# Kernel tuning notes

Measured on AMD Instinct MI355X. Metric: run time of the kernel, lower is better.

Reference implementation:

```python
import jax, jax.numpy as jnp
import numpy as np

T, B, D, H = 1024, 64, 128, 512
ALPHA = 10.0 / 100.0  # dt / tau


def setup_inputs() -> dict:
    key = jax.random.key(0)
    k1, k2, k3 = jax.random.split(key, 3)
    # scale weights modestly so relu recurrence stays stable
    inp = {
        "input": jax.random.normal(k1, (T, B, D), dtype=jnp.float32),
        "W_in": jax.random.normal(k2, (H, D), dtype=jnp.float32) * 0.05,
        "b_in": jnp.zeros((H,), dtype=jnp.float32),
        "W_hid": jax.random.normal(k3, (H, H), dtype=jnp.float32) * 0.05,
        "b_hid": jnp.zeros((H,), dtype=jnp.float32),
    }
    return inp


def reference(input, W_in, b_in, W_hid, b_hid):
    # Precompute input projection for all timesteps in one big GEMM: [T,B,H]
    w_in_u = jnp.einsum("tbd,hd->tbh", input, W_in) + b_in

    v0 = jnp.zeros((B, H), dtype=input.dtype)
    fr0 = jax.nn.relu(v0)

    def step(carry, w_in_u_t):
        fr_t, v_t = carry
        w_hid_fr = jnp.einsum("bh,gh->bg", fr_t, W_hid) + b_hid  # [B,H]
        v_t = (1.0 - ALPHA) * v_t + ALPHA * (w_hid_fr + w_in_u_t)
        fr_t = jax.nn.relu(v_t)
        return (fr_t, v_t), fr_t

    _, stacked = jax.lax.scan(step, (fr0, v0), w_in_u)
    return stacked  # [T, B, H]
```

## Files before the change

kernel.cpp:

```cpp
#include <hip/hip_runtime.h>
#include <stdint.h>

#define NT 1024
#define NB 64
#define ND 128
#define NH 512
#define NPAIR (NH / 2)

typedef float f32x4  __attribute__((ext_vector_type(4)));
typedef short bf16x8 __attribute__((ext_vector_type(8)));
typedef unsigned int uint32x4 __attribute__((ext_vector_type(4)));
typedef unsigned long long u64;

__device__ __forceinline__ unsigned short f2bf(float f) {
  uint32_t u = __float_as_uint(f);
  u += 0x7fffu + ((u >> 16) & 1u);
  return (unsigned short)(u >> 16);
}

__device__ __forceinline__ bf16x8 cvt8(f32x4 a, f32x4 b) {
  bf16x8 r;
  r[0] = (short)f2bf(a[0]); r[1] = (short)f2bf(a[1]);
  r[2] = (short)f2bf(a[2]); r[3] = (short)f2bf(a[3]);
  r[4] = (short)f2bf(b[0]); r[5] = (short)f2bf(b[1]);
  r[6] = (short)f2bf(b[2]); r[7] = (short)f2bf(b[3]);
  return r;
}

__device__ __forceinline__ void load_group(const u64* __restrict__ base, int g,
                                           u64* u) {
#pragma unroll
  for (int i = 0; i < 16; ++i)
    u[i] = __hip_atomic_load(base + g * 64 + (i >> 2) * 16 + (i & 3),
                             __ATOMIC_RELAXED, __HIP_MEMORY_SCOPE_AGENT);
}

__global__ __launch_bounds__(256, 1) void rnn_persistent(
    const float* __restrict__ input,
    const float* __restrict__ W_in,
    const float* __restrict__ b_in,
    const float* __restrict__ W_hid,
    const float* __restrict__ b_hid,
    float* __restrict__ out,
    u64* __restrict__ llbuf)
{
  __shared__ uint32x4 lds[2][16][64];

  const int wg   = blockIdx.x;
  const int rg   = wg >> 3;
  const int cg   = wg & 7;
  const int tid  = threadIdx.x;
  const int wv   = tid >> 6;
  const int lane = tid & 63;
  const int col  = lane & 15;
  const int quad = lane >> 4;
  const int kq   = quad * 8;

  const int bA = rg * 16 + col;
  const int gB = cg * 64 + wv * 16 + col;
  const int bC = rg * 16 + quad * 4;

  bf16x8 Bh[16];
#pragma unroll
  for (int kk = 0; kk < 16; ++kk) {
    const float* p = W_hid + (size_t)gB * NH + kk * 32 + kq;
    Bh[kk] = cvt8(*(const f32x4*)p, *(const f32x4*)(p + 4));
  }
  bf16x8 Bi[4];
#pragma unroll
  for (int kk = 0; kk < 4; ++kk) {
    const float* p = W_in + (size_t)gB * ND + kk * 32 + kq;
    Bi[kk] = cvt8(*(const f32x4*)p, *(const f32x4*)(p + 4));
  }
  const float blane = b_hid[gB] + b_in[gB];

  float v0 = 0.f, v1 = 0.f, v2 = 0.f, v3 = 0.f;
  u64 ua[16];

#pragma unroll 1
  for (int t = 0; t < NT; ++t) {
    const float* ip = input + ((size_t)t * NB + bA) * ND + kq;
    f32x4 x0 = *(const f32x4*)(ip);
    f32x4 x1 = *(const f32x4*)(ip + 4);
    f32x4 x2 = *(const f32x4*)(ip + 32);
    f32x4 x3 = *(const f32x4*)(ip + 36);
    f32x4 x4 = *(const f32x4*)(ip + 64);
    f32x4 x5 = *(const f32x4*)(ip + 68);
    f32x4 x6 = *(const f32x4*)(ip + 96);
    f32x4 x7 = *(const f32x4*)(ip + 100);

    const u64* cbase =
        llbuf + (size_t)((t & 1) * NB + bA) * NPAIR + quad * 4;

    if (t > 0) load_group(cbase, wv, ua);

    f32x4 acc = {0.f, 0.f, 0.f, 0.f};
    acc = __builtin_amdgcn_mfma_f32_16x16x32_bf16(cvt8(x0, x1), Bi[0], acc, 0, 0, 0);
    acc = __builtin_amdgcn_mfma_f32_16x16x32_bf16(cvt8(x2, x3), Bi[1], acc, 0, 0, 0);
    acc = __builtin_amdgcn_mfma_f32_16x16x32_bf16(cvt8(x4, x5), Bi[2], acc, 0, 0, 0);
    acc = __builtin_amdgcn_mfma_f32_16x16x32_bf16(cvt8(x6, x7), Bi[3], acc, 0, 0, 0);

    if (t > 0) {
      for (;;) {
        uint32_t m = 0;
#pragma unroll
        for (int i = 0; i < 16; ++i)
          m |= (uint32_t)(ua[i] >> 32) ^ (uint32_t)t;
        if (m == 0) break;
        __builtin_amdgcn_s_sleep(1);
        load_group(cbase, wv, ua);
      }
#pragma unroll
      for (int c = 0; c < 4; ++c) {
        uint32x4 p = {(uint32_t)ua[c * 4 + 0], (uint32_t)ua[c * 4 + 1],
                      (uint32_t)ua[c * 4 + 2], (uint32_t)ua[c * 4 + 3]};
        lds[t & 1][wv * 4 + c][lane] = p;
      }
      __syncthreads();
#pragma unroll
      for (int kk = 0; kk < 16; ++kk) {
        uint32x4 p = lds[t & 1][kk][lane];
        acc = __builtin_amdgcn_mfma_f32_16x16x32_bf16(
            __builtin_bit_cast(bf16x8, p), Bh[kk], acc, 0, 0, 0);
      }
    }

    v0 = 0.9f * v0 + 0.1f * (acc[0] + blane);
    v1 = 0.9f * v1 + 0.1f * (acc[1] + blane);
    v2 = 0.9f * v2 + 0.1f * (acc[2] + blane);
    v3 = 0.9f * v3 + 0.1f * (acc[3] + blane);
    float f0 = fmaxf(v0, 0.f), f1 = fmaxf(v1, 0.f);
    float f2 = fmaxf(v2, 0.f), f3 = fmaxf(v3, 0.f);

    float* op = out + ((size_t)t * NB + bC) * NH + gB;
    op[0]      = f0;
    op[NH]     = f1;
    op[2 * NH] = f2;
    op[3 * NH] = f3;

    float p0 = __shfl_xor(f0, 1, 64);
    float p1 = __shfl_xor(f1, 1, 64);
    float p2 = __shfl_xor(f2, 1, 64);
    float p3 = __shfl_xor(f3, 1, 64);
    if (!(lane & 1)) {
      const u64 tagw = ((u64)(uint32_t)(t + 1)) << 32;
      u64* pb = llbuf + (size_t)(((t + 1) & 1) * NB + bC) * NPAIR + (gB >> 1);
      u64 w0 = tagw | (u64)((uint32_t)f2bf(f0) | ((uint32_t)f2bf(p0) << 16));
      u64 w1 = tagw | (u64)((uint32_t)f2bf(f1) | ((uint32_t)f2bf(p1) << 16));
      u64 w2 = tagw | (u64)((uint32_t)f2bf(f2) | ((uint32_t)f2bf(p2) << 16));
      u64 w3 = tagw | (u64)((uint32_t)f2bf(f3) | ((uint32_t)f2bf(p3) << 16));
      __hip_atomic_store(pb + 0 * NPAIR, w0, __ATOMIC_RELAXED, __HIP_MEMORY_SCOPE_AGENT);
      __hip_atomic_store(pb + 1 * NPAIR, w1, __ATOMIC_RELAXED, __HIP_MEMORY_SCOPE_AGENT);
      __hip_atomic_store(pb + 2 * NPAIR, w2, __ATOMIC_RELAXED, __HIP_MEMORY_SCOPE_AGENT);
      __hip_atomic_store(pb + 3 * NPAIR, w3, __ATOMIC_RELAXED, __HIP_MEMORY_SCOPE_AGENT);
    }
  }
}

extern "C" void kernel_launch(void* const* d_in, const int* in_sizes, int n_in,
                              void* d_out, int out_size, void* d_ws, size_t ws_size,
                              hipStream_t stream) {
  const float* input = (const float*)d_in[0];
  const float* W_in  = (const float*)d_in[1];
  const float* b_in  = (const float*)d_in[2];
  const float* W_hid = (const float*)d_in[3];
  const float* b_hid = (const float*)d_in[4];
  float* out = (float*)d_out;

  u64* llbuf = (u64*)d_ws;

  hipLaunchKernelGGL(rnn_persistent, dim3(32), dim3(256), 0, stream,
                     input, W_in, b_in, W_hid, b_hid, out, llbuf);
}
```

Before: 4.412 ms.

## Use 8 blocks of 1024 threads with a coalesced handoff buffer layout

The persistent RNN now runs as 8 workgroups of 16 waves each, where before it used 32 workgroups of 4 waves. Each workgroup covers 256 hidden columns, so fewer blocks take part in the per-step cross-block handoff. The handoff buffer is laid out so that each consumer lane polls only 4 contiguous 64-bit words, down from 16, and producers write to matching slots. A bounded spin with a 'dead' flag is added so a hang cannot stall forever. The cost is larger blocks with heavier per-step __syncthreads across 16 waves.

```diff
diff --git a/kernel.cpp b/kernel.cpp
--- a/kernel.cpp
+++ b/kernel.cpp
@@ -5,7 +5,6 @@
 #define NB 64
 #define ND 128
 #define NH 512
-#define NPAIR (NH / 2)
 
 typedef float f32x4  __attribute__((ext_vector_type(4)));
 typedef short bf16x8 __attribute__((ext_vector_type(8)));
@@ -27,15 +26,7 @@
   return r;
 }
 
-__device__ __forceinline__ void load_group(const u64* __restrict__ base, int g,
-                                           u64* u) {
-#pragma unroll
-  for (int i = 0; i < 16; ++i)
-    u[i] = __hip_atomic_load(base + g * 64 + (i >> 2) * 16 + (i & 3),
-                             __ATOMIC_RELAXED, __HIP_MEMORY_SCOPE_AGENT);
-}
-
-__global__ __launch_bounds__(256, 1) void rnn_persistent(
+__global__ __launch_bounds__(1024, 1) void rnn_persistent(
     const float* __restrict__ input,
     const float* __restrict__ W_in,
     const float* __restrict__ b_in,
@@ -47,8 +38,8 @@
   __shared__ uint32x4 lds[2][16][64];
 
   const int wg   = blockIdx.x;
-  const int rg   = wg >> 3;
-  const int cg   = wg & 7;
+  const int rg   = wg >> 1;
+  const int cgh  = wg & 1;
   const int tid  = threadIdx.x;
   const int wv   = tid >> 6;
   const int lane = tid & 63;
@@ -57,7 +48,7 @@
   const int kq   = quad * 8;
 
   const int bA = rg * 16 + col;
-  const int gB = cg * 64 + wv * 16 + col;
+  const int gB = cgh * 256 + wv * 16 + col;
   const int bC = rg * 16 + quad * 4;
 
   bf16x8 Bh[16];
@@ -74,11 +65,26 @@
   }
   const float blane = b_hid[gB] + b_in[gB];
 
+  const u64* cons0 = llbuf + (size_t)((rg * 16 + wv) * 256 + lane);
+  const int P = cgh * 128 + wv * 8 + (col >> 1);
+  u64* prod0 = llbuf + (size_t)(((rg * 16 + (P >> 4)) * 4 + (P & 3)) * 64 +
+                                ((P >> 2) & 3) * 16 + quad * 4);
+
   float v0 = 0.f, v1 = 0.f, v2 = 0.f, v3 = 0.f;
-  u64 ua[16];
+  u64 u0 = 0, u1 = 0, u2 = 0, u3 = 0;
+  int dead = 0;
 
 #pragma unroll 1
   for (int t = 0; t < NT; ++t) {
+    const u64* cb = cons0 + (size_t)(t & 1) * 16384;
+
+    if (t > 0) {
+      u0 = __hip_atomic_load(cb,       __ATOMIC_RELAXED, __HIP_MEMORY_SCOPE_AGENT);
+      u1 = __hip_atomic_load(cb + 64,  __ATOMIC_RELAXED, __HIP_MEMORY_SCOPE_AGENT);
+      u2 = __hip_atomic_load(cb + 128, __ATOMIC_RELAXED, __HIP_MEMORY_SCOPE_AGENT);
+      u3 = __hip_atomic_load(cb + 192, __ATOMIC_RELAXED, __HIP_MEMORY_SCOPE_AGENT);
+    }
+
     const float* ip = input + ((size_t)t * NB + bA) * ND + kq;
     f32x4 x0 = *(const f32x4*)(ip);
     f32x4 x1 = *(const f32x4*)(ip + 4);
@@ -89,11 +95,6 @@
     f32x4 x6 = *(const f32x4*)(ip + 96);
     f32x4 x7 = *(const f32x4*)(ip + 100);
 
-    const u64* cbase =
-        llbuf + (size_t)((t & 1) * NB + bA) * NPAIR + quad * 4;
-
-    if (t > 0) load_group(cbase, wv, ua);
-
     f32x4 acc = {0.f, 0.f, 0.f, 0.f};
     acc = __builtin_amdgcn_mfma_f32_16x16x32_bf16(cvt8(x0, x1), Bi[0], acc, 0, 0, 0);
     acc = __builtin_amdgcn_mfma_f32_16x16x32_bf16(cvt8(x2, x3), Bi[1], acc, 0, 0, 0);
@@ -101,21 +102,24 @@
     acc = __builtin_amdgcn_mfma_f32_16x16x32_bf16(cvt8(x6, x7), Bi[3], acc, 0, 0, 0);
 
     if (t > 0) {
-      for (;;) {
-        uint32_t m = 0;
-#pragma unroll
-        for (int i = 0; i < 16; ++i)
-          m |= (uint32_t)(ua[i] >> 32) ^ (uint32_t)t;
-        if (m == 0) break;
+      const int lim = dead ? 0 : (1 << 20);
+      int tries = 0;
+      while ((((uint32_t)(u0 >> 32) ^ (uint32_t)t) |
+              ((uint32_t)(u1 >> 32) ^ (uint32_t)t) |
+              ((uint32_t)(u2 >> 32) ^ (uint32_t)t) |
+              ((uint32_t)(u3 >> 32) ^ (uint32_t)t)) != 0 &&
+             tries < lim) {
+        ++tries;
         __builtin_amdgcn_s_sleep(1);
-        load_group(cbase, wv, ua);
+        u0 = __hip_atomic_load(cb,       __ATOMIC_RELAXED, __HIP_MEMORY_SCOPE_AGENT);
+        u1 = __hip_atomic_load(cb + 64,  __ATOMIC_RELAXED, __HIP_MEMORY_SCOPE_AGENT);
+        u2 = __hip_atomic_load(cb + 128, __ATOMIC_RELAXED, __HIP_MEMORY_SCOPE_AGENT);
+        u3 = __hip_atomic_load(cb + 192, __ATOMIC_RELAXED, __HIP_MEMORY_SCOPE_AGENT);
       }
-#pragma unroll
-      for (int c = 0; c < 4; ++c) {
-        uint32x4 p = {(uint32_t)ua[c * 4 + 0], (uint32_t)ua[c * 4 + 1],
-                      (uint32_t)ua[c * 4 + 2], (uint32_t)ua[c * 4 + 3]};
-        lds[t & 1][wv * 4 + c][lane] = p;
-      }
+      if (tries >= (1 << 20)) dead = 1;
+
+      uint32x4 pay = {(uint32_t)u0, (uint32_t)u1, (uint32_t)u2, (uint32_t)u3};
+      lds[t & 1][wv][lane] = pay;
       __syncthreads();
 #pragma unroll
       for (int kk = 0; kk < 16; ++kk) {
@@ -144,15 +148,15 @@
     float p3 = __shfl_xor(f3, 1, 64);
     if (!(lane & 1)) {
       const u64 tagw = ((u64)(uint32_t)(t + 1)) << 32;
-      u64* pb = llbuf + (size_t)(((t + 1) & 1) * NB + bC) * NPAIR + (gB >> 1);
       u64 w0 = tagw | (u64)((uint32_t)f2bf(f0) | ((uint32_t)f2bf(p0) << 16));
       u64 w1 = tagw | (u64)((uint32_t)f2bf(f1) | ((uint32_t)f2bf(p1) << 16));
       u64 w2 = tagw | (u64)((uint32_t)f2bf(f2) | ((uint32_t)f2bf(p2) << 16));
       u64 w3 = tagw | (u64)((uint32_t)f2bf(f3) | ((uint32_t)f2bf(p3) << 16));
-      __hip_atomic_store(pb + 0 * NPAIR, w0, __ATOMIC_RELAXED, __HIP_MEMORY_SCOPE_AGENT);
-      __hip_atomic_store(pb + 1 * NPAIR, w1, __ATOMIC_RELAXED, __HIP_MEMORY_SCOPE_AGENT);
-      __hip_atomic_store(pb + 2 * NPAIR, w2, __ATOMIC_RELAXED, __HIP_MEMORY_SCOPE_AGENT);
-      __hip_atomic_store(pb + 3 * NPAIR, w3, __ATOMIC_RELAXED, __HIP_MEMORY_SCOPE_AGENT);
+      u64* pb = prod0 + (size_t)((t + 1) & 1) * 16384;
+      __hip_atomic_store(pb,     w0, __ATOMIC_RELAXED, __HIP_MEMORY_SCOPE_AGENT);
+      __hip_atomic_store(pb + 1, w1, __ATOMIC_RELAXED, __HIP_MEMORY_SCOPE_AGENT);
+      __hip_atomic_store(pb + 2, w2, __ATOMIC_RELAXED, __HIP_MEMORY_SCOPE_AGENT);
+      __hip_atomic_store(pb + 3, w3, __ATOMIC_RELAXED, __HIP_MEMORY_SCOPE_AGENT);
     }
   }
 }
@@ -169,6 +173,6 @@
 
   u64* llbuf = (u64*)d_ws;
 
-  hipLaunchKernelGGL(rnn_persistent, dim3(32), dim3(256), 0, stream,
+  hipLaunchKernelGGL(rnn_persistent, dim3(8), dim3(1024), 0, stream,
                      input, W_in, b_in, W_hid, b_hid, out, llbuf);
 }
```

Measured after the change: 9.225 ms. 2.09x slower.
